# Optimization experiments

Hardware: AMD Instinct MI355X
Metric: run time of the kernel (lower is better)

The kernel has to match this reference:

```python
import jax, jax.numpy as jnp
import numpy as np

NUM_HEADS = 32
NUM_KV_GROUPS = 8
HEAD_DIM = 64  # dim_out // num_heads
DIM_IN = 2048
DIM_OUT = 2048


def setup_inputs() -> dict:
    key = jax.random.key(0)
    k_x, k_q, k_k, k_v, k_o = jax.random.split(key, 5)
    s = 0.02
    x = jax.random.normal(k_x, (1, 2048, DIM_IN), dtype=jnp.float32)
    wq = jax.random.normal(k_q, (DIM_IN, DIM_OUT), dtype=jnp.float32) * s
    wk = jax.random.normal(k_k, (DIM_IN, NUM_KV_GROUPS * HEAD_DIM), dtype=jnp.float32) * s
    wv = jax.random.normal(k_v, (DIM_IN, NUM_KV_GROUPS * HEAD_DIM), dtype=jnp.float32) * s
    wo = jax.random.normal(k_o, (DIM_OUT, DIM_OUT), dtype=jnp.float32) * s
    return {"x": x, "wq": wq, "wk": wk, "wv": wv, "wo": wo}


def reference(x, wq, wk, wv, wo):
    b, n, _ = x.shape
    g, r, d = NUM_KV_GROUPS, NUM_HEADS // NUM_KV_GROUPS, HEAD_DIM
    # projections
    q = (x @ wq).reshape(b, n, g, r, d)          # [b,n,g,r,d] heads grouped
    k = (x @ wk).reshape(b, n, g, d)             # [b,n,g,d]
    v = (x @ wv).reshape(b, n, g, d)
    # scores: repeat_interleave of K over group dim == broadcast over r
    scores = jnp.einsum('bqgrd,bkgd->bgrqk', q, k)  # [b,g,r,n,n]
    causal = jnp.tril(jnp.ones((n, n), dtype=bool))
    scores = jnp.where(causal, scores, -jnp.inf)
    attn = jax.nn.softmax(scores / jnp.sqrt(jnp.asarray(d, x.dtype)), axis=-1)
    ctx = jnp.einsum('bgrqk,bkgd->bqgrd', attn, v)  # [b,n,g,r,d]
    out = ctx.reshape(b, n, g * r * d) @ wo
    return out
```

## Files before the change

### kernel.cpp

```cpp
#include <hip/hip_runtime.h>


typedef __attribute__((ext_vector_type(8))) short bf16x8;
typedef __attribute__((ext_vector_type(4))) short bf16x4;
typedef __attribute__((ext_vector_type(4))) float f32x4;
typedef __attribute__((ext_vector_type(4))) unsigned u32x4;

__device__ __forceinline__ short f2bf(float f) {
  unsigned u = __builtin_bit_cast(unsigned, f);
  u += 0x7FFFu + ((u >> 16) & 1u);
  return (short)(u >> 16);
}

__device__ __forceinline__ unsigned pkbf(float a, float b) {
  const unsigned ua = __builtin_bit_cast(unsigned, a) + 0x8000u;
  const unsigned ub = __builtin_bit_cast(unsigned, b) + 0x8000u;
  return __builtin_amdgcn_perm(ub, ua, 0x07060302u);
}

__device__ __forceinline__ void pswap(unsigned a, unsigned b,
                                      unsigned& r0, unsigned& r1) {
  auto t = __builtin_amdgcn_permlane32_swap(a, b, false, false);
  auto u = __builtin_amdgcn_permlane16_swap(t[0], t[1], false, false);
  r0 = u[0]; r1 = u[1];
}

__device__ __forceinline__ void build_bfrag(const f32x4* sv, bf16x8& b0, bf16x8& b1) {
  const unsigned c0 = pkbf(sv[0][0], sv[0][1]), d0 = pkbf(sv[0][2], sv[0][3]);
  const unsigned c1 = pkbf(sv[1][0], sv[1][1]), d1 = pkbf(sv[1][2], sv[1][3]);
  const unsigned c2 = pkbf(sv[2][0], sv[2][1]), d2 = pkbf(sv[2][2], sv[2][3]);
  const unsigned c3 = pkbf(sv[3][0], sv[3][1]), d3 = pkbf(sv[3][2], sv[3][3]);
  unsigned q0, q1, q2, q3, r0, r1, r2, r3;
  pswap(c0, c1, q0, q2); pswap(d0, d1, q1, q3);
  pswap(c2, c3, r0, r2); pswap(d2, d3, r1, r3);
  b0 = __builtin_bit_cast(bf16x8, (u32x4){q0, q1, q2, q3});
  b1 = __builtin_bit_cast(bf16x8, (u32x4){r0, r1, r2, r3});
}

__device__ __forceinline__ void gload_lds16(const void* g, void* l) {
  __builtin_amdgcn_global_load_lds(
      (const __attribute__((address_space(1))) unsigned int*)g,
      (__attribute__((address_space(3))) unsigned int*)l, 16, 0, 0);
}

__global__ __launch_bounds__(256) void tcvt4(const float* __restrict__ wq,
                                             const float* __restrict__ wk,
                                             const float* __restrict__ wv,
                                             const float* __restrict__ wo,
                                             const float* __restrict__ x,
                                             short* __restrict__ dq,
                                             short* __restrict__ dk,
                                             short* __restrict__ dv,
                                             short* __restrict__ dwo,
                                             short* __restrict__ xb) {
  const int z = blockIdx.z;
  if (z == 4) {
    const int id = blockIdx.y * gridDim.x + blockIdx.x;
    const int i = (id * 256 + threadIdx.x) * 4;
    const float4 v = *(const float4*)&x[i];
    bf16x4 r;
    r[0] = f2bf(v.x); r[1] = f2bf(v.y); r[2] = f2bf(v.z); r[3] = f2bf(v.w);
    *(bf16x4*)&xb[i] = r;
    return;
  }
  const float* src;
  short* dst;
  int C;
  if (z == 0)      { src = wq; dst = dq;  C = 2048; }
  else if (z == 1) { src = wk; dst = dk;  C = 512; }
  else if (z == 2) { src = wv; dst = dv;  C = 512; }
  else             { src = wo; dst = dwo; C = 2048; }
  const int c0 = blockIdx.x * 32;
  if (c0 >= C) return;
  const int R = 2048;
  __shared__ float t[32][33];
  const int r0 = blockIdx.y * 32;
  const int tx = threadIdx.x & 31, ty = threadIdx.x >> 5;
#pragma unroll
  for (int i = 0; i < 4; ++i)
    t[ty + i * 8][tx] = src[(r0 + ty + i * 8) * C + c0 + tx];
  __syncthreads();
#pragma unroll
  for (int i = 0; i < 4; ++i)
    dst[(c0 + ty + i * 8) * R + r0 + tx] = f2bf(t[tx][ty + i * 8]);
}

__global__ __launch_bounds__(256) void tbf(const short* __restrict__ src,
                                           short* __restrict__ dst,
                                           int R, int C, int ldsrc) {
  __shared__ short t[32][33];
  const int c0 = blockIdx.x * 32, r0 = blockIdx.y * 32;
  const int tx = threadIdx.x & 31, ty = threadIdx.x >> 5;
#pragma unroll
  for (int i = 0; i < 4; ++i)
    t[ty + i * 8][tx] = src[(r0 + ty + i * 8) * ldsrc + c0 + tx];
  __syncthreads();
#pragma unroll
  for (int i = 0; i < 4; ++i)
    dst[(c0 + ty + i * 8) * R + r0 + tx] = t[tx][ty + i * 8];
}

template <int OUT_BF16, int BN>
__global__ __launch_bounds__(256) void gemm_bt(const short* __restrict__ A,
                                               const short* __restrict__ B,
                                               void* __restrict__ Cv,
                                               int M, int N, int K,
                                               float cscale, int scale_cols) {
  constexpr int NF = BN / 32;
  __shared__ short As[2][128 * 64];
  __shared__ short Bs[2][BN * 64];
  const int tid = threadIdx.x;
  const int lane = tid & 63, wid = tid >> 6;
  const int l15 = lane & 15, lg = lane >> 4;
  const int lr8 = lane >> 3, lc8 = lane & 7;
  const int wr = wid >> 1, wc = wid & 1;
  const int nx = gridDim.x;
  const int orig = blockIdx.y * nx + blockIdx.x;
  const int nwg = nx * gridDim.y;
  const int wgid = (orig & 7) * (nwg >> 3) + (orig >> 3);
  const int bx = wgid % nx, by = wgid / nx;
  const int row0 = by * 128, col0 = bx * BN;
  const int sswz = l15 & 7;
  f32x4 acc[4][NF] = {};
  const short* ag = A + (row0 + wid * 32 + lr8) * K + (lc8 ^ lr8) * 8;
  const short* bg = B + (col0 + wid * NF * 8 + lr8) * K + (lc8 ^ lr8) * 8;

  auto stage = [&](int b, int kk) {
    short* lA = &As[b][wid * 2048];
    short* lB = &Bs[b][wid * NF * 512];
#pragma unroll
    for (int c = 0; c < 4; ++c)
      gload_lds16(ag + c * 8 * K + kk, lA + c * 512);
#pragma unroll
    for (int c = 0; c < NF; ++c)
      gload_lds16(bg + c * 8 * K + kk, lB + c * 512);
  };

  stage(0, 0);
  __syncthreads();
  const int nb = K / 64;
  int buf = 0;
  for (int t = 0; t < nb; ++t) {
    if (t + 1 < nb) stage(buf ^ 1, (t + 1) * 64);
#pragma unroll
    for (int x = 0; x < 2; ++x) {
      bf16x8 af[4], bfr[NF];
#pragma unroll
      for (int m = 0; m < 4; ++m)
        af[m] = *(const bf16x8*)&As[buf][(wr * 64 + m * 16 + l15) * 64 + (((x * 4 + lg) ^ sswz) * 8)];
#pragma unroll
      for (int n = 0; n < NF; ++n)
        bfr[n] = *(const bf16x8*)&Bs[buf][(wc * (BN / 2) + n * 16 + l15) * 64 + (((x * 4 + lg) ^ sswz) * 8)];
#pragma unroll
      for (int m = 0; m < 4; ++m)
#pragma unroll
        for (int n = 0; n < NF; ++n)
          acc[m][n] = __builtin_amdgcn_mfma_f32_16x16x32_bf16(af[m], bfr[n],
                                                              acc[m][n], 0, 0, 0);
    }
    __syncthreads();
    buf ^= 1;
  }
#pragma unroll
  for (int m = 0; m < 4; ++m)
#pragma unroll
    for (int n = 0; n < NF; ++n)
#pragma unroll
      for (int i = 0; i < 4; ++i) {
        const int r = row0 + wr * 64 + m * 16 + lg * 4 + i;
        const int c = col0 + wc * (BN / 2) + n * 16 + l15;
        float v = acc[m][n][i];
        if (c < scale_cols) v *= cscale;
        if (OUT_BF16)
          ((short*)Cv)[r * N + c] = f2bf(v);
        else
          ((float*)Cv)[r * N + c] = v;
      }
}

__global__ __launch_bounds__(512) void attn_fwd(const short* __restrict__ QKV,
                                                const short* __restrict__ Vt,
                                                short* __restrict__ CTX) {
  const int ldq = 3072;
  const int hp = blockIdx.x;
  const int bxp = blockIdx.y;
  const int g = hp >> 1;
  const int h0 = g * 4 + (hp & 1) * 2;
  const int tid = threadIdx.x;
  const int lane = tid & 63, wid = tid >> 6;
  const int grp = wid >> 2;
  const int wq = wid & 3;
  const int l15 = lane & 15, lg = lane >> 4;

  __shared__ short Ks[2][2][64 * 64];
  __shared__ short Vs[2][2][64 * 64];
  __shared__ float CB[4][64][36];

  const int ltid = tid & 255;
  const int srow = ltid >> 3, sseg = ltid & 7;
  const int ssw = (sseg ^ (srow & 7)) * 8;
  const short* Kg = QKV + 2048 + g * 64 + sseg * 8;
  const short* Vg = Vt + (g * 64 + srow) * 2048 + sseg * 8;

  bf16x8 rk0, rk1, rv0, rv1;
  {
    const int tb = grp * 64;
    rk0 = *(const bf16x8*)&Kg[(tb + srow) * ldq];
    rk1 = *(const bf16x8*)&Kg[(tb + srow + 32) * ldq];
    rv0 = *(const bf16x8*)&Vg[tb];
    rv1 = *(const bf16x8*)&Vg[32 * 2048 + tb];
  }

#pragma unroll 1
  for (int half = 0; half < 2; ++half) {
    const int qb = half ? bxp : 31 - bxp;
    const int qrow0 = qb * 64 + wq * 16;

    bf16x8 qf[2][2];
#pragma unroll
    for (int hh = 0; hh < 2; ++hh)
#pragma unroll
      for (int kc = 0; kc < 2; ++kc)
        qf[hh][kc] = *(const bf16x8*)&QKV[(qrow0 + l15) * ldq + (h0 + hh) * 64 + kc * 32 + lg * 8];

    float l_run[2] = {0.f, 0.f};
    f32x4 accO[2][4] = {};

    const int nint = (qb >> 1) + 1;
#pragma unroll 1
    for (int j = 0; j < nint; ++j) {
      const int kt = 2 * j + grp;
      const bool valid = kt <= qb;
      const int buf = j & 1;
      if (valid) {
        *(bf16x8*)&Ks[grp][buf][srow * 64 + ssw] = rk0;
        *(bf16x8*)&Ks[grp][buf][(srow + 32) * 64 + ssw] = rk1;
        *(bf16x8*)&Vs[grp][buf][srow * 64 + ssw] = rv0;
        *(bf16x8*)&Vs[grp][buf][(srow + 32) * 64 + ssw] = rv1;
      }
      if (kt + 2 <= qb) {
        const int nb = (kt + 2) * 64;
        rk0 = *(const bf16x8*)&Kg[(nb + srow) * ldq];
        rk1 = *(const bf16x8*)&Kg[(nb + srow + 32) * ldq];
        rv0 = *(const bf16x8*)&Vg[nb];
        rv1 = *(const bf16x8*)&Vg[32 * 2048 + nb];
      }
      __syncthreads();
      if (!valid) continue;

      const int tokbase = kt * 64;
      f32x4 s[2][4];
      __builtin_amdgcn_s_setprio(1);
#pragma unroll
      for (int t = 0; t < 4; ++t) {
        s[0][t] = (f32x4){0.f, 0.f, 0.f, 0.f};
        s[1][t] = (f32x4){0.f, 0.f, 0.f, 0.f};
#pragma unroll
        for (int kc = 0; kc < 2; ++kc) {
          const bf16x8 kf =
              *(const bf16x8*)&Ks[grp][buf][(t * 16 + l15) * 64 + (((kc * 4 + lg) ^ (l15 & 7)) * 8)];
          s[0][t] = __builtin_amdgcn_mfma_f32_16x16x32_bf16(kf, qf[0][kc], s[0][t], 0, 0, 0);
          s[1][t] = __builtin_amdgcn_mfma_f32_16x16x32_bf16(kf, qf[1][kc], s[1][t], 0, 0, 0);
        }
      }
      __builtin_amdgcn_s_setprio(0);

      if (kt == qb) {
        const int kq = tokbase + lg * 4 - qrow0 - l15;
#pragma unroll
        for (int t = 0; t < 4; ++t)
#pragma unroll
          for (int i = 0; i < 4; ++i)
            if (kq + t * 16 + i > 0) { s[0][t][i] = -3e38f; s[1][t][i] = -3e38f; }
      }

#pragma unroll
      for (int hh = 0; hh < 2; ++hh) {
        float ts = 0.f;
#pragma unroll
        for (int t = 0; t < 4; ++t) {
          const float e0 = __builtin_amdgcn_exp2f(s[hh][t][0]);
          const float e1 = __builtin_amdgcn_exp2f(s[hh][t][1]);
          const float e2 = __builtin_amdgcn_exp2f(s[hh][t][2]);
          const float e3 = __builtin_amdgcn_exp2f(s[hh][t][3]);
          s[hh][t][0] = e0; s[hh][t][1] = e1; s[hh][t][2] = e2; s[hh][t][3] = e3;
          ts += (e0 + e1) + (e2 + e3);
        }
        ts += __shfl_xor(ts, 16);
        ts += __shfl_xor(ts, 32);
        l_run[hh] += ts;
      }

      bf16x8 pb[2][2];
      build_bfrag(s[0], pb[0][0], pb[0][1]);
      build_bfrag(s[1], pb[1][0], pb[1][1]);

      __builtin_amdgcn_s_setprio(1);
#pragma unroll
      for (int kc = 0; kc < 2; ++kc)
#pragma unroll
        for (int t2 = 0; t2 < 4; ++t2) {
          const bf16x8 vb =
              *(const bf16x8*)&Vs[grp][buf][(t2 * 16 + l15) * 64 + (((kc * 4 + lg) ^ (l15 & 7)) * 8)];
          accO[0][t2] = __builtin_amdgcn_mfma_f32_16x16x32_bf16(vb, pb[0][kc], accO[0][t2], 0, 0, 0);
          accO[1][t2] = __builtin_amdgcn_mfma_f32_16x16x32_bf16(vb, pb[1][kc], accO[1][t2], 0, 0, 0);
        }
      __builtin_amdgcn_s_setprio(0);
    }

    if (half == 0 && grp <= bxp) {
      const int tb = grp * 64;
      rk0 = *(const bf16x8*)&Kg[(tb + srow) * ldq];
      rk1 = *(const bf16x8*)&Kg[(tb + srow + 32) * ldq];
      rv0 = *(const bf16x8*)&Vg[tb];
      rv1 = *(const bf16x8*)&Vg[32 * 2048 + tb];
    }

    if (grp == 1) {
#pragma unroll
      for (int hh = 0; hh < 2; ++hh)
#pragma unroll
        for (int t2 = 0; t2 < 4; ++t2)
          *(f32x4*)&CB[wq][lane][hh * 16 + t2 * 4] = accO[hh][t2];
      *(float2*)&CB[wq][lane][32] = make_float2(l_run[0], l_run[1]);
    }
    __syncthreads();
    if (grp == 0) {
      const float2 lcb = *(const float2*)&CB[wq][lane][32];
#pragma unroll
      for (int hh = 0; hh < 2; ++hh) {
        const float lt = l_run[hh] + (hh ? lcb.y : lcb.x);
        const float inv = 1.0f / lt;
        f32x4 ov[4];
#pragma unroll
        for (int t2 = 0; t2 < 4; ++t2) {
          const f32x4 cb = *(const f32x4*)&CB[wq][lane][hh * 16 + t2 * 4];
#pragma unroll
          for (int i = 0; i < 4; ++i) ov[t2][i] = (accO[hh][t2][i] + cb[i]) * inv;
        }
        bf16x8 ob0, ob1;
        build_bfrag(ov, ob0, ob1);
        *(bf16x8*)&CTX[(qrow0 + l15) * 2048 + (h0 + hh) * 64 + lg * 8] = ob0;
        *(bf16x8*)&CTX[(qrow0 + l15) * 2048 + (h0 + hh) * 64 + 32 + lg * 8] = ob1;
      }
    }
  }
}

extern "C" void kernel_launch(void* const* d_in, const int* in_sizes, int n_in,
                              void* d_out, int out_size, void* d_ws, size_t ws_size,
                              hipStream_t stream) {
  (void)in_sizes; (void)n_in; (void)out_size; (void)ws_size;
  const float* x  = (const float*)d_in[0];
  const float* wq = (const float*)d_in[1];
  const float* wk = (const float*)d_in[2];
  const float* wv = (const float*)d_in[3];
  const float* wo = (const float*)d_in[4];
  float* out = (float*)d_out;

  char* ws = (char*)d_ws;
  short* Xb  = (short*)(ws);
  short* WT  = (short*)(ws + 8388608);
  short* WoT = (short*)(ws + 20971520);
  short* QKV = (short*)(ws + 29360128);
  short* Vt  = (short*)(ws + 41943040);
  short* CTX = (short*)(ws + 44040192);

  const float qscale = 0.125f * 1.4426950408889634f;

  { dim3 g(64, 64, 5);
    tcvt4<<<g, 256, 0, stream>>>(wq, wk, wv, wo, x,
                                 WT, WT + 2048 * 2048, WT + 2560 * 2048, WoT, Xb); }
  { dim3 g(32, 16);
    gemm_bt<1, 96><<<g, 256, 0, stream>>>(Xb, WT, QKV, 2048, 3072, 2048,
                                          qscale, 2048); }
  { dim3 g(16, 64); tbf<<<g, 256, 0, stream>>>(QKV + 2560, Vt, 2048, 512, 3072); }
  { dim3 g(16, 16); attn_fwd<<<g, 512, 0, stream>>>(QKV, Vt, CTX); }
  { dim3 g(32, 16);
    gemm_bt<0, 64><<<g, 256, 0, stream>>>(CTX, WoT, out, 2048, 2048, 2048,
                                          1.0f, 0); }
}
```

Measured before the change: 117.1 us.

## Stage K/V tiles with direct global-to-LDS loads and restructure double buffering

Replaces the register-staged K/V prefetch (global to VGPR, then ds_write) with direct global-to-LDS loads issued one tile ahead into the alternate buffer. The compute body moves inside the valid branch, with a single barrier at the end of each iteration. The goal is to free VGPRs, drop the LDS write instructions, and overlap the next tile's fetch with MFMA work. It depends on gload_lds16 completion being correctly ordered by the barrier, and the swizzle now comes from the per-lane source address.

```diff
diff --git a/kernel.cpp b/kernel.cpp
--- a/kernel.cpp
+++ b/kernel.cpp
@@ -196,20 +196,22 @@
   __shared__ short Vs[2][2][64 * 64];
   __shared__ float CB[4][64][36];
 
-  const int ltid = tid & 255;
-  const int srow = ltid >> 3, sseg = ltid & 7;
-  const int ssw = (sseg ^ (srow & 7)) * 8;
-  const short* Kg = QKV + 2048 + g * 64 + sseg * 8;
-  const short* Vg = Vt + (g * 64 + srow) * 2048 + sseg * 8;
-
-  bf16x8 rk0, rk1, rv0, rv1;
-  {
-    const int tb = grp * 64;
-    rk0 = *(const bf16x8*)&Kg[(tb + srow) * ldq];
-    rk1 = *(const bf16x8*)&Kg[(tb + srow + 32) * ldq];
-    rv0 = *(const bf16x8*)&Vg[tb];
-    rv1 = *(const bf16x8*)&Vg[32 * 2048 + tb];
-  }
+  const int wl = wid & 3;
+  const int l8 = lane >> 3, s8 = lane & 7;
+  const int r0 = wl * 8 + l8;
+  const int csw = (s8 ^ (r0 & 7)) * 8;
+  const short* Kga = QKV + 2048 + g * 64 + csw;
+  const short* Vga = Vt + (g * 64 + r0) * 2048 + csw;
+
+  auto stageKV = [&](int buf, int tokbase) {
+    gload_lds16(Kga + (tokbase + r0) * ldq,      &Ks[grp][buf][wl * 512]);
+    gload_lds16(Kga + (tokbase + r0 + 32) * ldq, &Ks[grp][buf][2048 + wl * 512]);
+    gload_lds16(Vga + tokbase,                   &Vs[grp][buf][wl * 512]);
+    gload_lds16(Vga + 32 * 2048 + tokbase,       &Vs[grp][buf][2048 + wl * 512]);
+  };
+
+  stageKV(0, grp * 64);
+  __syncthreads();
 
 #pragma unroll 1
   for (int half = 0; half < 2; ++half) {
@@ -232,89 +234,71 @@
       const int kt = 2 * j + grp;
       const bool valid = kt <= qb;
       const int buf = j & 1;
+      if (kt + 2 <= qb) stageKV(buf ^ 1, (kt + 2) * 64);
       if (valid) {
-        *(bf16x8*)&Ks[grp][buf][srow * 64 + ssw] = rk0;
-        *(bf16x8*)&Ks[grp][buf][(srow + 32) * 64 + ssw] = rk1;
-        *(bf16x8*)&Vs[grp][buf][srow * 64 + ssw] = rv0;
-        *(bf16x8*)&Vs[grp][buf][(srow + 32) * 64 + ssw] = rv1;
-      }
-      if (kt + 2 <= qb) {
-        const int nb = (kt + 2) * 64;
-        rk0 = *(const bf16x8*)&Kg[(nb + srow) * ldq];
-        rk1 = *(const bf16x8*)&Kg[(nb + srow + 32) * ldq];
-        rv0 = *(const bf16x8*)&Vg[nb];
-        rv1 = *(const bf16x8*)&Vg[32 * 2048 + nb];
+        const int tokbase = kt * 64;
+        f32x4 s[2][4];
+        __builtin_amdgcn_s_setprio(1);
+#pragma unroll
+        for (int t = 0; t < 4; ++t) {
+          s[0][t] = (f32x4){0.f, 0.f, 0.f, 0.f};
+          s[1][t] = (f32x4){0.f, 0.f, 0.f, 0.f};
+#pragma unroll
+          for (int kc = 0; kc < 2; ++kc) {
+            const bf16x8 kf =
+                *(const bf16x8*)&Ks[grp][buf][(t * 16 + l15) * 64 + (((kc * 4 + lg) ^ (l15 & 7)) * 8)];
+            s[0][t] = __builtin_amdgcn_mfma_f32_16x16x32_bf16(kf, qf[0][kc], s[0][t], 0, 0, 0);
+            s[1][t] = __builtin_amdgcn_mfma_f32_16x16x32_bf16(kf, qf[1][kc], s[1][t], 0, 0, 0);
+          }
+        }
+        __builtin_amdgcn_s_setprio(0);
+
+        if (kt == qb) {
+          const int kq = tokbase + lg * 4 - qrow0 - l15;
+#pragma unroll
+          for (int t = 0; t < 4; ++t)
+#pragma unroll
+            for (int i = 0; i < 4; ++i)
+              if (kq + t * 16 + i > 0) { s[0][t][i] = -3e38f; s[1][t][i] = -3e38f; }
+        }
+
+#pragma unroll
+        for (int hh = 0; hh < 2; ++hh) {
+          float ts = 0.f;
+#pragma unroll
+          for (int t = 0; t < 4; ++t) {
+            const float e0 = __builtin_amdgcn_exp2f(s[hh][t][0]);
+            const float e1 = __builtin_amdgcn_exp2f(s[hh][t][1]);
+            const float e2 = __builtin_amdgcn_exp2f(s[hh][t][2]);
+            const float e3 = __builtin_amdgcn_exp2f(s[hh][t][3]);
+            s[hh][t][0] = e0; s[hh][t][1] = e1; s[hh][t][2] = e2; s[hh][t][3] = e3;
+            ts += (e0 + e1) + (e2 + e3);
+          }
+          ts += __shfl_xor(ts, 16);
+          ts += __shfl_xor(ts, 32);
+          l_run[hh] += ts;
+        }
+
+        bf16x8 pb[2][2];
+        build_bfrag(s[0], pb[0][0], pb[0][1]);
+        build_bfrag(s[1], pb[1][0], pb[1][1]);
+
+        __builtin_amdgcn_s_setprio(1);
+#pragma unroll
+        for (int kc = 0; kc < 2; ++kc)
+#pragma unroll
+          for (int t2 = 0; t2 < 4; ++t2) {
+            const bf16x8 vb =
+                *(const bf16x8*)&Vs[grp][buf][(t2 * 16 + l15) * 64 + (((kc * 4 + lg) ^ (l15 & 7)) * 8)];
+            accO[0][t2] = __builtin_amdgcn_mfma_f32_16x16x32_bf16(vb, pb[0][kc], accO[0][t2], 0, 0, 0);
+            accO[1][t2] = __builtin_amdgcn_mfma_f32_16x16x32_bf16(vb, pb[1][kc], accO[1][t2], 0, 0, 0);
+          }
+        __builtin_amdgcn_s_setprio(0);
       }
       __syncthreads();
-      if (!valid) continue;
-
-      const int tokbase = kt * 64;
-      f32x4 s[2][4];
-      __builtin_amdgcn_s_setprio(1);
-#pragma unroll
-      for (int t = 0; t < 4; ++t) {
-        s[0][t] = (f32x4){0.f, 0.f, 0.f, 0.f};
-        s[1][t] = (f32x4){0.f, 0.f, 0.f, 0.f};
-#pragma unroll
-        for (int kc = 0; kc < 2; ++kc) {
-          const bf16x8 kf =
-              *(const bf16x8*)&Ks[grp][buf][(t * 16 + l15) * 64 + (((kc * 4 + lg) ^ (l15 & 7)) * 8)];
-          s[0][t] = __builtin_amdgcn_mfma_f32_16x16x32_bf16(kf, qf[0][kc], s[0][t], 0, 0, 0);
-          s[1][t] = __builtin_amdgcn_mfma_f32_16x16x32_bf16(kf, qf[1][kc], s[1][t], 0, 0, 0);
-        }
-      }
-      __builtin_amdgcn_s_setprio(0);
-
-      if (kt == qb) {
-        const int kq = tokbase + lg * 4 - qrow0 - l15;
-#pragma unroll
-        for (int t = 0; t < 4; ++t)
-#pragma unroll
-          for (int i = 0; i < 4; ++i)
-            if (kq + t * 16 + i > 0) { s[0][t][i] = -3e38f; s[1][t][i] = -3e38f; }
-      }
-
-#pragma unroll
-      for (int hh = 0; hh < 2; ++hh) {
-        float ts = 0.f;
-#pragma unroll
-        for (int t = 0; t < 4; ++t) {
-          const float e0 = __builtin_amdgcn_exp2f(s[hh][t][0]);
-          const float e1 = __builtin_amdgcn_exp2f(s[hh][t][1]);
-          const float e2 = __builtin_amdgcn_exp2f(s[hh][t][2]);
-          const float e3 = __builtin_amdgcn_exp2f(s[hh][t][3]);
-          s[hh][t][0] = e0; s[hh][t][1] = e1; s[hh][t][2] = e2; s[hh][t][3] = e3;
-          ts += (e0 + e1) + (e2 + e3);
-        }
-        ts += __shfl_xor(ts, 16);
-        ts += __shfl_xor(ts, 32);
-        l_run[hh] += ts;
-      }
-
-      bf16x8 pb[2][2];
-      build_bfrag(s[0], pb[0][0], pb[0][1]);
-      build_bfrag(s[1], pb[1][0], pb[1][1]);
-
-      __builtin_amdgcn_s_setprio(1);
-#pragma unroll
-      for (int kc = 0; kc < 2; ++kc)
-#pragma unroll
-        for (int t2 = 0; t2 < 4; ++t2) {
-          const bf16x8 vb =
-              *(const bf16x8*)&Vs[grp][buf][(t2 * 16 + l15) * 64 + (((kc * 4 + lg) ^ (l15 & 7)) * 8)];
-          accO[0][t2] = __builtin_amdgcn_mfma_f32_16x16x32_bf16(vb, pb[0][kc], accO[0][t2], 0, 0, 0);
-          accO[1][t2] = __builtin_amdgcn_mfma_f32_16x16x32_bf16(vb, pb[1][kc], accO[1][t2], 0, 0, 0);
-        }
-      __builtin_amdgcn_s_setprio(0);
     }
 
-    if (half == 0 && grp <= bxp) {
-      const int tb = grp * 64;
-      rk0 = *(const bf16x8*)&Kg[(tb + srow) * ldq];
-      rk1 = *(const bf16x8*)&Kg[(tb + srow + 32) * ldq];
-      rv0 = *(const bf16x8*)&Vg[tb];
-      rv1 = *(const bf16x8*)&Vg[32 * 2048 + tb];
-    }
+    if (half == 0 && grp <= bxp) stageKV(0, grp * 64);
 
     if (grp == 1) {
 #pragma unroll
```

After: 121.4 us. 1.04x slower.

## Replace direct global-to-LDS loads with register-staged prefetch and one barrier per tile

Applied to the files above, without the earlier changes.

The GEMM kernel stops using global_load_lds and instead prefetches the next K-tile into registers, writes it to a double-buffered shared tile, and synchronizes with a single LDS-only barrier per iteration instead of two __syncthreads. The attention kernel's barrier is also replaced with a barrier that waits only on LDS counters, so the register prefetch of K/V does not have to complete before the barrier, and a __syncthreads is added at the end of the outer loop. The aim is to cut barrier and vmcnt stalls so the global loads overlap with MFMA work, at the cost of more registers and extra LDS store instructions. Correctness with a single barrier per iteration relies on the double buffer keeping writes to one buffer apart from reads of the other.

```diff
diff --git a/kernel.cpp b/kernel.cpp
--- a/kernel.cpp
+++ b/kernel.cpp
@@ -37,10 +37,9 @@
   b1 = __builtin_bit_cast(bf16x8, (u32x4){r0, r1, r2, r3});
 }
 
-__device__ __forceinline__ void gload_lds16(const void* g, void* l) {
-  __builtin_amdgcn_global_load_lds(
-      (const __attribute__((address_space(1))) unsigned int*)g,
-      (__attribute__((address_space(3))) unsigned int*)l, 16, 0, 0);
+__device__ __forceinline__ void lds_barrier() {
+  asm volatile("s_waitcnt lgkmcnt(0)" ::: "memory");
+  __builtin_amdgcn_s_barrier();
 }
 
 __global__ __launch_bounds__(256) void tcvt4(const float* __restrict__ wq,
@@ -121,27 +120,34 @@
   const int bx = wgid % nx, by = wgid / nx;
   const int row0 = by * 128, col0 = bx * BN;
   const int sswz = l15 & 7;
+  const int wswz = (lc8 ^ lr8) * 8;
   f32x4 acc[4][NF] = {};
-  const short* ag = A + (row0 + wid * 32 + lr8) * K + (lc8 ^ lr8) * 8;
-  const short* bg = B + (col0 + wid * NF * 8 + lr8) * K + (lc8 ^ lr8) * 8;
-
-  auto stage = [&](int b, int kk) {
-    short* lA = &As[b][wid * 2048];
-    short* lB = &Bs[b][wid * NF * 512];
-#pragma unroll
-    for (int c = 0; c < 4; ++c)
-      gload_lds16(ag + c * 8 * K + kk, lA + c * 512);
-#pragma unroll
-    for (int c = 0; c < NF; ++c)
-      gload_lds16(bg + c * 8 * K + kk, lB + c * 512);
-  };
-
-  stage(0, 0);
-  __syncthreads();
+  const short* ag = A + (row0 + wid * 32 + lr8) * K + lc8 * 8;
+  const short* bg = B + (col0 + wid * NF * 8 + lr8) * K + lc8 * 8;
+
+  bf16x8 ra[4], rb[NF];
+#pragma unroll
+  for (int c = 0; c < 4; ++c) ra[c] = *(const bf16x8*)&ag[c * 8 * K];
+#pragma unroll
+  for (int c = 0; c < NF; ++c) rb[c] = *(const bf16x8*)&bg[c * 8 * K];
+
   const int nb = K / 64;
   int buf = 0;
   for (int t = 0; t < nb; ++t) {
-    if (t + 1 < nb) stage(buf ^ 1, (t + 1) * 64);
+#pragma unroll
+    for (int c = 0; c < 4; ++c)
+      *(bf16x8*)&As[buf][(wid * 32 + c * 8 + lr8) * 64 + wswz] = ra[c];
+#pragma unroll
+    for (int c = 0; c < NF; ++c)
+      *(bf16x8*)&Bs[buf][(wid * NF * 8 + c * 8 + lr8) * 64 + wswz] = rb[c];
+    if (t + 1 < nb) {
+      const int kk = (t + 1) * 64;
+#pragma unroll
+      for (int c = 0; c < 4; ++c) ra[c] = *(const bf16x8*)&ag[c * 8 * K + kk];
+#pragma unroll
+      for (int c = 0; c < NF; ++c) rb[c] = *(const bf16x8*)&bg[c * 8 * K + kk];
+    }
+    lds_barrier();
 #pragma unroll
     for (int x = 0; x < 2; ++x) {
       bf16x8 af[4], bfr[NF];
@@ -158,7 +164,6 @@
           acc[m][n] = __builtin_amdgcn_mfma_f32_16x16x32_bf16(af[m], bfr[n],
                                                               acc[m][n], 0, 0, 0);
     }
-    __syncthreads();
     buf ^= 1;
   }
 #pragma unroll
@@ -245,7 +250,7 @@
         rv0 = *(const bf16x8*)&Vg[nb];
         rv1 = *(const bf16x8*)&Vg[32 * 2048 + nb];
       }
-      __syncthreads();
+      lds_barrier();
       if (!valid) continue;
 
       const int tokbase = kt * 64;
@@ -344,6 +349,7 @@
         *(bf16x8*)&CTX[(qrow0 + l15) * 2048 + (h0 + hh) * 64 + 32 + lg * 8] = ob1;
       }
     }
+    __syncthreads();
   }
 }
 
```

After: 114.9 us. Within noise of the previous version (-1.9%).
